# Optimization experiments

Measured on AMD Instinct MI355X. Metric: run time of the kernel, lower is better.

The kernel has to match this reference:

```python
import jax, jax.numpy as jnp
import numpy as np

B, C, D, H, W = 2, 256, 16, 64, 64


def _conv1x1(x, w, b):
    # 1x1x1 Conv3d == pointwise channel matmul. x: [B,C,D,H,W], w: [Cout,Cin], b: [Cout]
    return jnp.einsum('bcdhw,oc->bodhw', x, w) + b[None, :, None, None, None]


def setup_inputs() -> dict:
    key = jax.random.key(0)
    ks = jax.random.split(key, 12)
    wscale = 1.0 / np.sqrt(C)  # keep pre-softmax logits in a sane range
    inp = {
        'eeg_input': jax.random.normal(ks[0], (B, C, D, H, W), jnp.float32),
        'image_input': jax.random.normal(ks[1], (B, C, D, H, W), jnp.float32),
        'q_w': jax.random.normal(ks[2], (C, C), jnp.float32) * wscale,
        'q_b': jnp.zeros((C,), jnp.float32),
        'k_w': jax.random.normal(ks[3], (C, C), jnp.float32) * wscale,
        'k_b': jnp.zeros((C,), jnp.float32),
        'v_w': jax.random.normal(ks[4], (C, C), jnp.float32) * wscale,
        'v_b': jnp.zeros((C,), jnp.float32),
        'attn_w': jax.random.normal(ks[5], (C, C), jnp.float32) * wscale,
        'attn_b': jnp.zeros((C,), jnp.float32),
        'out_w': jax.random.normal(ks[6], (C, C), jnp.float32) * wscale,
        'out_b': jnp.zeros((C,), jnp.float32),
    }
    return inp


def reference(eeg_input, image_input, q_w, q_b, k_w, k_b, v_w, v_b,
              attn_w, attn_b, out_w, out_b):
    q = _conv1x1(eeg_input, q_w, q_b)      # [B,C,D,H,W]
    k = _conv1x1(image_input, k_w, k_b)    # [B,C,D,H,W]
    v = _conv1x1(image_input, v_w, v_b)    # [B,C,D,H,W]
    # torch.matmul(q, k.transpose(-2,-1)): contract over W -> scores [B,C,D,H,H]
    scores = jax.nn.softmax(jnp.einsum('bcdhw,bcdxw->bcdhx', q, k), axis=-1)
    wv = jnp.einsum('bcdhx,bcdxw->bcdhw', scores, v)  # [B,C,D,H,W]
    a = jax.nn.relu(_conv1x1(wv, attn_w, attn_b))
    return jax.nn.relu(_conv1x1(a, out_w, out_b))
```

## Files before the change

### kernel.cpp

```cpp
#include <hip/hip_runtime.h>

#define CC   256
#define DHWC 65536
#define NBC  2

typedef __attribute__((ext_vector_type(8))) short bf16x8;
typedef __attribute__((ext_vector_type(4))) short bf16x4;
typedef __attribute__((ext_vector_type(4))) float f32x4;

__device__ __forceinline__ short f2bf(float x) {
    unsigned u = __builtin_bit_cast(unsigned, x);
    unsigned r = (u + 0x7fffu + ((u >> 16) & 1u)) >> 16;
    return (short)r;
}
__device__ __forceinline__ float bf2f(short h) {
    unsigned u = ((unsigned)(unsigned short)h) << 16;
    return __builtin_bit_cast(float, u);
}

__device__ __forceinline__ int swz(int r, int c) {
    return (r * 128 + c * 2) ^ ((r & 7) << 4);
}
__device__ __forceinline__ int swz512(int s, int k) {
    return (s * 512 + k * 2) ^ ((s & 7) << 4);
}

__global__ void prep_w_kernel(const float* __restrict__ q_w, const float* __restrict__ k_w,
                              const float* __restrict__ v_w, const float* __restrict__ attn_w,
                              const float* __restrict__ out_w, short* __restrict__ wsp)
{
    const int l  = threadIdx.x;
    const int fo = blockIdx.x;
    const int t  = blockIdx.y;
    const int m  = blockIdx.z;
    const float* w = (m == 0) ? q_w : (m == 1) ? k_w : (m == 2) ? v_w
                   : (m == 3) ? attn_w : out_w;
    short* whi = wsp + (size_t)m * 2 * 65536;
    short* wlo = whi + 65536;

    const int o = fo * 16 + (l & 15);
    const int k = t * 32 + (l >> 4) * 8;

    bf16x8 hv, lv;
    #pragma unroll
    for (int r = 0; r < 8; ++r) {
        const float x = w[o * 256 + k + r];
        const short h = f2bf(x);
        hv[r] = h;
        lv[r] = f2bf(x - bf2f(h));
    }
    const int idx = (fo * 8 + t) * 64 + l;
    *(bf16x8*)(whi + idx * 8) = hv;
    *(bf16x8*)(wlo + idx * 8) = lv;
}

__global__ __launch_bounds__(512, 4) void conv_mfma_kernel(
    const float* __restrict__ x, const short* __restrict__ whi,
    const short* __restrict__ wlo, const float* __restrict__ bias,
    float* __restrict__ out, const int do_relu)
{
    __shared__ bf16x8 xhi[2][512];
    __shared__ bf16x8 xlo[2][512];

    const int tid  = threadIdx.x;
    const int lane = tid & 63;
    const int wave = tid >> 6;
    const size_t boff = (size_t)blockIdx.y * ((size_t)CC * DHWC);
    const int sT = blockIdx.x * 64;
    const float* xb = x + boff + sT;
    const bf16x8* whf = (const bf16x8*)whi;
    const bf16x8* wlf = (const bf16x8*)wlo;

    f32x4 acc[2][4];
    #pragma unroll
    for (int f = 0; f < 2; ++f)
        #pragma unroll
        for (int j = 0; j < 4; ++j)
            acc[f][j] = (f32x4){0.f, 0.f, 0.f, 0.f};

    const int s_l = tid & 63;
    const int k8  = tid >> 6;

    float xr[8];
    #pragma unroll
    for (int r = 0; r < 8; ++r)
        xr[r] = xb[(size_t)(k8 * 8 + r) * DHWC + s_l];
    {
        bf16x8 hv, lv;
        #pragma unroll
        for (int r = 0; r < 8; ++r) {
            const short h = f2bf(xr[r]);
            hv[r] = h;
            lv[r] = f2bf(xr[r] - bf2f(h));
        }
        *(bf16x8*)((char*)xhi[0] + swz(s_l, k8 * 8)) = hv;
        *(bf16x8*)((char*)xlo[0] + swz(s_l, k8 * 8)) = lv;
    }

    #pragma unroll
    for (int t = 0; t < 4; ++t) {
        if (t < 3) {
            #pragma unroll
            for (int r = 0; r < 8; ++r)
                xr[r] = xb[(size_t)((t + 1) * 64 + k8 * 8 + r) * DHWC + s_l];
        }
        __syncthreads();

        const char* bhib = (const char*)xhi[t & 1];
        const char* blob = (const char*)xlo[t & 1];
        #pragma unroll
        for (int kk = 0; kk < 2; ++kk) {
            bf16x8 a1h[2], a1l[2];
            #pragma unroll
            for (int f = 0; f < 2; ++f) {
                const int idx = ((wave * 2 + f) * 8 + 2 * t + kk) * 64 + lane;
                a1h[f] = whf[idx];
                a1l[f] = wlf[idx];
            }
            bf16x8 bh[4], bl[4];
            #pragma unroll
            for (int j = 0; j < 4; ++j) {
                const int s = j * 16 + (lane & 15);
                const int k = kk * 32 + (lane >> 4) * 8;
                bh[j] = *(const bf16x8*)(bhib + swz(s, k));
                bl[j] = *(const bf16x8*)(blob + swz(s, k));
            }
            #pragma unroll
            for (int f = 0; f < 2; ++f)
                #pragma unroll
                for (int j = 0; j < 4; ++j) {
                    f32x4 c = acc[f][j];
                    c = __builtin_amdgcn_mfma_f32_16x16x32_bf16(a1h[f], bh[j], c, 0, 0, 0);
                    c = __builtin_amdgcn_mfma_f32_16x16x32_bf16(a1h[f], bl[j], c, 0, 0, 0);
                    c = __builtin_amdgcn_mfma_f32_16x16x32_bf16(a1l[f], bh[j], c, 0, 0, 0);
                    acc[f][j] = c;
                }
        }

        if (t < 3) {
            bf16x8 hv, lv;
            #pragma unroll
            for (int r = 0; r < 8; ++r) {
                const short h = f2bf(xr[r]);
                hv[r] = h;
                lv[r] = f2bf(xr[r] - bf2f(h));
            }
            *(bf16x8*)((char*)xhi[(t + 1) & 1] + swz(s_l, k8 * 8)) = hv;
            *(bf16x8*)((char*)xlo[(t + 1) & 1] + swz(s_l, k8 * 8)) = lv;
        }
    }

    float* ob = out + boff + sT;
    const int n_l = lane & 15;
    const int m4  = (lane >> 4) * 4;
    #pragma unroll
    for (int f = 0; f < 2; ++f) {
        #pragma unroll
        for (int r = 0; r < 4; ++r) {
            const int o = wave * 32 + f * 16 + m4 + r;
            const float bv = bias[o];
            #pragma unroll
            for (int j = 0; j < 4; ++j) {
                float val = acc[f][j][r] + bv;
                if (do_relu) val = fmaxf(val, 0.f);
                ob[(size_t)o * DHWC + j * 16 + n_l] = val;
            }
        }
    }
}

__global__ __launch_bounds__(256, 4) void attn_mfma_kernel(
    const float* __restrict__ q, const float* __restrict__ kg,
    const float* __restrict__ v, float* __restrict__ wv)
{
    __shared__ char lds[40960];
    const int QHI = 0, QLO = 8192, KHI = 16384, KLO = 24576, VTHI = 32768;

    const int tid  = threadIdx.x;
    const int lane = tid & 63;
    const int wsx  = tid >> 6;
    const size_t base = (size_t)blockIdx.x * 4096;

    {
        const int r  = tid >> 2;
        const int cb = (tid & 3) * 16;
        #pragma unroll
        for (int half = 0; half < 2; ++half) {
            const int c = cb + half * 8;
            const float4 qa = *(const float4*)(q  + base + r * 64 + c);
            const float4 qb = *(const float4*)(q  + base + r * 64 + c + 4);
            const float4 ka = *(const float4*)(kg + base + r * 64 + c);
            const float4 kb = *(const float4*)(kg + base + r * 64 + c + 4);
            bf16x8 qh, ql, kh, kl;
            #pragma unroll
            for (int e = 0; e < 4; ++e) {
                float xq = ((const float*)&qa)[e];
                short h = f2bf(xq); qh[e] = h; ql[e] = f2bf(xq - bf2f(h));
                xq = ((const float*)&qb)[e];
                h = f2bf(xq); qh[e + 4] = h; ql[e + 4] = f2bf(xq - bf2f(h));
                float xk = ((const float*)&ka)[e];
                h = f2bf(xk); kh[e] = h; kl[e] = f2bf(xk - bf2f(h));
                xk = ((const float*)&kb)[e];
                h = f2bf(xk); kh[e + 4] = h; kl[e + 4] = f2bf(xk - bf2f(h));
            }
            const int off = swz(r, c);
            *(bf16x8*)(lds + QHI + off) = qh;
            *(bf16x8*)(lds + QLO + off) = ql;
            *(bf16x8*)(lds + KHI + off) = kh;
            *(bf16x8*)(lds + KLO + off) = kl;
        }
        const int x0 = (tid >> 4) * 4;
        const int w0 = (tid & 15) * 4;
        float4 vr[4];
        #pragma unroll
        for (int i = 0; i < 4; ++i)
            vr[i] = *(const float4*)(v + base + (size_t)(x0 + i) * 64 + w0);
        #pragma unroll
        for (int j = 0; j < 4; ++j) {
            bf16x4 h4;
            #pragma unroll
            for (int i = 0; i < 4; ++i)
                h4[i] = f2bf(((const float*)&vr[i])[j]);
            *(bf16x4*)(lds + VTHI + swz(w0 + j, x0)) = h4;
        }
    }
    __syncthreads();

    f32x4 acc[4];
    #pragma unroll
    for (int j = 0; j < 4; ++j) acc[j] = (f32x4){0.f, 0.f, 0.f, 0.f};

    const int arow = wsx * 16 + (lane & 15);
    #pragma unroll
    for (int kk = 0; kk < 2; ++kk) {
        const int kcol = kk * 32 + (lane >> 4) * 8;
        const bf16x8 aqh = *(const bf16x8*)(lds + QHI + swz(arow, kcol));
        const bf16x8 aql = *(const bf16x8*)(lds + QLO + swz(arow, kcol));
        #pragma unroll
        for (int j = 0; j < 4; ++j) {
            const int brow = j * 16 + (lane & 15);
            const bf16x8 bkh = *(const bf16x8*)(lds + KHI + swz(brow, kcol));
            const bf16x8 bkl = *(const bf16x8*)(lds + KLO + swz(brow, kcol));
            f32x4 c = acc[j];
            c = __builtin_amdgcn_mfma_f32_16x16x32_bf16(aqh, bkh, c, 0, 0, 0);
            c = __builtin_amdgcn_mfma_f32_16x16x32_bf16(aqh, bkl, c, 0, 0, 0);
            c = __builtin_amdgcn_mfma_f32_16x16x32_bf16(aql, bkh, c, 0, 0, 0);
            acc[j] = c;
        }
    }

    float p[4][4], invs[4];
    #pragma unroll
    for (int r = 0; r < 4; ++r) {
        float m = fmaxf(fmaxf(acc[0][r], acc[1][r]), fmaxf(acc[2][r], acc[3][r]));
        m = fmaxf(m, __shfl_xor(m, 1));
        m = fmaxf(m, __shfl_xor(m, 2));
        m = fmaxf(m, __shfl_xor(m, 4));
        m = fmaxf(m, __shfl_xor(m, 8));
        float s = 0.f;
        #pragma unroll
        for (int j = 0; j < 4; ++j) { p[j][r] = __expf(acc[j][r] - m); s += p[j][r]; }
        s += __shfl_xor(s, 1);
        s += __shfl_xor(s, 2);
        s += __shfl_xor(s, 4);
        s += __shfl_xor(s, 8);
        invs[r] = 1.f / s;
    }

    __syncthreads();

    #pragma unroll
    for (int r = 0; r < 4; ++r) {
        const int row = wsx * 16 + (lane >> 4) * 4 + r;
        #pragma unroll
        for (int j = 0; j < 4; ++j) {
            const int col = j * 16 + (lane & 15);
            *(short*)(lds + QHI + swz(row, col)) = f2bf(p[j][r]);
        }
    }
    __syncthreads();

    f32x4 o_[4];
    #pragma unroll
    for (int j = 0; j < 4; ++j) o_[j] = (f32x4){0.f, 0.f, 0.f, 0.f};

    #pragma unroll
    for (int kk = 0; kk < 2; ++kk) {
        const int kcol = kk * 32 + (lane >> 4) * 8;
        const bf16x8 aph = *(const bf16x8*)(lds + QHI + swz(arow, kcol));
        #pragma unroll
        for (int j = 0; j < 4; ++j) {
            const int brow = j * 16 + (lane & 15);
            const bf16x8 bvh = *(const bf16x8*)(lds + VTHI + swz(brow, kcol));
            o_[j] = __builtin_amdgcn_mfma_f32_16x16x32_bf16(aph, bvh, o_[j], 0, 0, 0);
        }
    }

    #pragma unroll
    for (int r = 0; r < 4; ++r) {
        const int h = wsx * 16 + (lane >> 4) * 4 + r;
        #pragma unroll
        for (int j = 0; j < 4; ++j)
            wv[base + (size_t)h * 64 + j * 16 + (lane & 15)] = o_[j][r] * invs[r];
    }
}

__global__ __launch_bounds__(512, 4) void tail_fused_kernel(
    const float* __restrict__ x,
    const short* __restrict__ w1hi, const short* __restrict__ w1lo,
    const float* __restrict__ b1,
    const short* __restrict__ w2hi, const short* __restrict__ w2lo,
    const float* __restrict__ b2,
    float* __restrict__ out)
{
    __shared__ char lds[65536];
    const int tid  = threadIdx.x;
    const int lane = tid & 63;
    const int wave = tid >> 6;
    const size_t boff = (size_t)blockIdx.y * ((size_t)CC * DHWC);
    const int sT = blockIdx.x * 64;
    const float* xb = x + boff + sT;
    const bf16x8* w1hf = (const bf16x8*)w1hi;
    const bf16x8* w1lf = (const bf16x8*)w1lo;

    f32x4 acc[2][4];
    #pragma unroll
    for (int f = 0; f < 2; ++f)
        #pragma unroll
        for (int j = 0; j < 4; ++j)
            acc[f][j] = (f32x4){0.f, 0.f, 0.f, 0.f};

    const int s_l = tid & 63;
    const int k8  = tid >> 6;

    float xr[8];
    #pragma unroll
    for (int r = 0; r < 8; ++r)
        xr[r] = xb[(size_t)(k8 * 8 + r) * DHWC + s_l];
    {
        bf16x8 hv, lv;
        #pragma unroll
        for (int r = 0; r < 8; ++r) {
            const short h = f2bf(xr[r]);
            hv[r] = h;
            lv[r] = f2bf(xr[r] - bf2f(h));
        }
        *(bf16x8*)(lds + swz(s_l, k8 * 8)) = hv;
        *(bf16x8*)(lds + 8192 + swz(s_l, k8 * 8)) = lv;
    }

    #pragma unroll
    for (int t = 0; t < 4; ++t) {
        if (t < 3) {
            #pragma unroll
            for (int r = 0; r < 8; ++r)
                xr[r] = xb[(size_t)((t + 1) * 64 + k8 * 8 + r) * DHWC + s_l];
        }
        __syncthreads();

        const char* bhib = lds + (t & 1) * 16384;
        const char* blob = bhib + 8192;
        #pragma unroll
        for (int kk = 0; kk < 2; ++kk) {
            bf16x8 a1h[2], a1l[2];
            #pragma unroll
            for (int f = 0; f < 2; ++f) {
                const int idx = ((wave * 2 + f) * 8 + 2 * t + kk) * 64 + lane;
                a1h[f] = w1hf[idx];
                a1l[f] = w1lf[idx];
            }
            bf16x8 bh[4], bl[4];
            #pragma unroll
            for (int j = 0; j < 4; ++j) {
                const int s = j * 16 + (lane & 15);
                const int k = kk * 32 + (lane >> 4) * 8;
                bh[j] = *(const bf16x8*)(bhib + swz(s, k));
                bl[j] = *(const bf16x8*)(blob + swz(s, k));
            }
            #pragma unroll
            for (int f = 0; f < 2; ++f)
                #pragma unroll
                for (int j = 0; j < 4; ++j) {
                    f32x4 c = acc[f][j];
                    c = __builtin_amdgcn_mfma_f32_16x16x32_bf16(a1h[f], bh[j], c, 0, 0, 0);
                    c = __builtin_amdgcn_mfma_f32_16x16x32_bf16(a1h[f], bl[j], c, 0, 0, 0);
                    c = __builtin_amdgcn_mfma_f32_16x16x32_bf16(a1l[f], bh[j], c, 0, 0, 0);
                    acc[f][j] = c;
                }
        }

        if (t < 3) {
            bf16x8 hv, lv;
            #pragma unroll
            for (int r = 0; r < 8; ++r) {
                const short h = f2bf(xr[r]);
                hv[r] = h;
                lv[r] = f2bf(xr[r] - bf2f(h));
            }
            *(bf16x8*)(lds + ((t + 1) & 1) * 16384 + swz(s_l, k8 * 8)) = hv;
            *(bf16x8*)(lds + ((t + 1) & 1) * 16384 + 8192 + swz(s_l, k8 * 8)) = lv;
        }
    }

    __syncthreads();
    #pragma unroll
    for (int f = 0; f < 2; ++f) {
        #pragma unroll
        for (int r = 0; r < 4; ++r) {
            const int o = wave * 32 + f * 16 + (lane >> 4) * 4 + r;
            const float bv = b1[o];
            #pragma unroll
            for (int j = 0; j < 4; ++j) {
                const int s = j * 16 + (lane & 15);
                const float val = fmaxf(acc[f][j][r] + bv, 0.f);
                const short h = f2bf(val);
                const int off = swz512(s, o);
                *(short*)(lds + off) = h;
                *(short*)(lds + 32768 + off) = f2bf(val - bf2f(h));
            }
        }
    }
    __syncthreads();

    f32x4 acc2[2][4];
    #pragma unroll
    for (int f = 0; f < 2; ++f)
        #pragma unroll
        for (int j = 0; j < 4; ++j)
            acc2[f][j] = (f32x4){0.f, 0.f, 0.f, 0.f};

    const bf16x8* w2hf = (const bf16x8*)w2hi;
    const bf16x8* w2lf = (const bf16x8*)w2lo;
    #pragma unroll
    for (int t2 = 0; t2 < 8; ++t2) {
        bf16x8 a2h[2], a2l[2];
        #pragma unroll
        for (int f = 0; f < 2; ++f) {
            const int idx = ((wave * 2 + f) * 8 + t2) * 64 + lane;
            a2h[f] = w2hf[idx];
            a2l[f] = w2lf[idx];
        }
        bf16x8 bh[4], bl[4];
        #pragma unroll
        for (int j = 0; j < 4; ++j) {
            const int s = j * 16 + (lane & 15);
            const int k = t2 * 32 + (lane >> 4) * 8;
            const int off = swz512(s, k);
            bh[j] = *(const bf16x8*)(lds + off);
            bl[j] = *(const bf16x8*)(lds + 32768 + off);
        }
        #pragma unroll
        for (int f = 0; f < 2; ++f)
            #pragma unroll
            for (int j = 0; j < 4; ++j) {
                f32x4 c = acc2[f][j];
                c = __builtin_amdgcn_mfma_f32_16x16x32_bf16(a2h[f], bh[j], c, 0, 0, 0);
                c = __builtin_amdgcn_mfma_f32_16x16x32_bf16(a2h[f], bl[j], c, 0, 0, 0);
                c = __builtin_amdgcn_mfma_f32_16x16x32_bf16(a2l[f], bh[j], c, 0, 0, 0);
                acc2[f][j] = c;
            }
    }

    float* ob = out + boff + sT;
    const int n_l = lane & 15;
    const int m4  = (lane >> 4) * 4;
    #pragma unroll
    for (int f = 0; f < 2; ++f) {
        #pragma unroll
        for (int r = 0; r < 4; ++r) {
            const int o = wave * 32 + f * 16 + m4 + r;
            const float bv = b2[o];
            #pragma unroll
            for (int j = 0; j < 4; ++j) {
                const float val = fmaxf(acc2[f][j][r] + bv, 0.f);
                ob[(size_t)o * DHWC + j * 16 + n_l] = val;
            }
        }
    }
}

extern "C" void kernel_launch(void* const* d_in, const int* in_sizes, int n_in,
                              void* d_out, int out_size, void* d_ws, size_t ws_size,
                              hipStream_t stream)
{
    const float* eeg    = (const float*)d_in[0];
    const float* img    = (const float*)d_in[1];
    const float* q_w    = (const float*)d_in[2];
    const float* q_b    = (const float*)d_in[3];
    const float* k_w    = (const float*)d_in[4];
    const float* k_b    = (const float*)d_in[5];
    const float* v_w    = (const float*)d_in[6];
    const float* v_b    = (const float*)d_in[7];
    const float* attn_w = (const float*)d_in[8];
    const float* attn_b = (const float*)d_in[9];
    const float* out_w  = (const float*)d_in[10];
    const float* out_b  = (const float*)d_in[11];

    float* outp = (float*)d_out;
    const size_t N = (size_t)NBC * CC * DHWC;
    float* qbuf = (float*)d_ws;
    float* kbuf = qbuf + N;
    short* wsp  = (short*)(kbuf + N);

    hipLaunchKernelGGL(prep_w_kernel, dim3(16, 8, 5), dim3(64), 0, stream,
                       q_w, k_w, v_w, attn_w, out_w, wsp);

    const dim3 cgrid(DHWC / 64, NBC);
    const dim3 cblk(512);
    #define WMAT(m) (wsp + (size_t)(m) * 2 * 65536), (wsp + (size_t)(m) * 2 * 65536 + 65536)

    hipLaunchKernelGGL(conv_mfma_kernel, cgrid, cblk, 0, stream, eeg,  WMAT(0), q_b, qbuf, 0);
    hipLaunchKernelGGL(conv_mfma_kernel, cgrid, cblk, 0, stream, img,  WMAT(1), k_b, kbuf, 0);
    hipLaunchKernelGGL(conv_mfma_kernel, cgrid, cblk, 0, stream, img,  WMAT(2), v_b, outp, 0);
    hipLaunchKernelGGL(attn_mfma_kernel, dim3(NBC * CC * 16), dim3(256), 0, stream,
                       qbuf, kbuf, outp, qbuf);
    hipLaunchKernelGGL(tail_fused_kernel, cgrid, cblk, 0, stream,
                       qbuf, WMAT(3), attn_b, WMAT(4), out_b, outp);
    #undef WMAT
}
```

Measured before the change: 438.8 us.

## Fuse QKV projections into one kernel and pass pre-split bf16 intermediates

The three separate conv kernels are merged into one qkv_kernel that stages each input tile in LDS once, so the image tile is shared between the K and V projections. Q and K are written as packed hi/lo bf16 pairs and V as plain bf16, which removes the float-to-bf16 splitting in the attention kernel and halves V traffic. The attention output is also written packed, so the tail kernel only unpacks it. In exchange, the non-double-buffered 64KB LDS staging lowers occupancy and loses the load/compute overlap the old conv kernels had. V is now stored at bf16 precision before attention, and the V transpose uses a new swizzle.

```diff
diff --git a/kernel.cpp b/kernel.cpp
--- a/kernel.cpp
+++ b/kernel.cpp
@@ -20,6 +20,9 @@
 
 __device__ __forceinline__ int swz(int r, int c) {
     return (r * 128 + c * 2) ^ ((r & 7) << 4);
+}
+__device__ __forceinline__ int vswz(int r, int c) {
+    return (r * 128 + c * 2) ^ (((r ^ (r >> 3)) & 7) << 4);
 }
 __device__ __forceinline__ int swz512(int s, int k) {
     return (s * 512 + k * 2) ^ ((s & 7) << 4);
@@ -35,7 +38,7 @@
     const int m  = blockIdx.z;
     const float* w = (m == 0) ? q_w : (m == 1) ? k_w : (m == 2) ? v_w
                    : (m == 3) ? attn_w : out_w;
-    short* whi = wsp + (size_t)m * 2 * 65536;
+    short* whi = wsp + (size_t)m * 131072;
     short* wlo = whi + 65536;
 
     const int o = fo * 16 + (l & 15);
@@ -54,127 +57,185 @@
     *(bf16x8*)(wlo + idx * 8) = lv;
 }
 
-__global__ __launch_bounds__(512, 4) void conv_mfma_kernel(
-    const float* __restrict__ x, const short* __restrict__ whi,
-    const short* __restrict__ wlo, const float* __restrict__ bias,
-    float* __restrict__ out, const int do_relu)
-{
-    __shared__ bf16x8 xhi[2][512];
-    __shared__ bf16x8 xlo[2][512];
-
+__device__ __forceinline__ void gemm256(const char* lds, const short* whi,
+                                        const short* wlo, int wave, int lane,
+                                        f32x4 acc[2][4])
+{
+    const bf16x8* whf = (const bf16x8*)whi;
+    const bf16x8* wlf = (const bf16x8*)wlo;
+    #pragma unroll
+    for (int t2 = 0; t2 < 8; ++t2) {
+        bf16x8 a2h[2], a2l[2];
+        #pragma unroll
+        for (int f = 0; f < 2; ++f) {
+            const int idx = ((wave * 2 + f) * 8 + t2) * 64 + lane;
+            a2h[f] = whf[idx];
+            a2l[f] = wlf[idx];
+        }
+        bf16x8 bh[4], bl[4];
+        #pragma unroll
+        for (int j = 0; j < 4; ++j) {
+            const int s = j * 16 + (lane & 15);
+            const int k = t2 * 32 + (lane >> 4) * 8;
+            const int off = swz512(s, k);
+            bh[j] = *(const bf16x8*)(lds + off);
+            bl[j] = *(const bf16x8*)(lds + 32768 + off);
+        }
+        #pragma unroll
+        for (int f = 0; f < 2; ++f)
+            #pragma unroll
+            for (int j = 0; j < 4; ++j) {
+                f32x4 c = acc[f][j];
+                c = __builtin_amdgcn_mfma_f32_16x16x32_bf16(a2h[f], bh[j], c, 0, 0, 0);
+                c = __builtin_amdgcn_mfma_f32_16x16x32_bf16(a2h[f], bl[j], c, 0, 0, 0);
+                c = __builtin_amdgcn_mfma_f32_16x16x32_bf16(a2l[f], bh[j], c, 0, 0, 0);
+                acc[f][j] = c;
+            }
+    }
+}
+
+__device__ __forceinline__ void stage_f32(const float* xb, char* lds, int tid)
+{
+    const int s_l = tid & 63;
+    const int k8  = tid >> 6;
+    #pragma unroll
+    for (int t = 0; t < 4; ++t) {
+        float xr[8];
+        #pragma unroll
+        for (int r = 0; r < 8; ++r)
+            xr[r] = xb[(size_t)(t * 64 + k8 * 8 + r) * DHWC + s_l];
+        bf16x8 hv, lv;
+        #pragma unroll
+        for (int r = 0; r < 8; ++r) {
+            const short h = f2bf(xr[r]);
+            hv[r] = h;
+            lv[r] = f2bf(xr[r] - bf2f(h));
+        }
+        const int off = swz512(s_l, t * 64 + k8 * 8);
+        *(bf16x8*)(lds + off) = hv;
+        *(bf16x8*)(lds + 32768 + off) = lv;
+    }
+}
+
+__device__ __forceinline__ void stage_u32(const unsigned* xb, char* lds, int tid)
+{
+    const int s_l = tid & 63;
+    const int k8  = tid >> 6;
+    #pragma unroll
+    for (int t = 0; t < 4; ++t) {
+        unsigned xu[8];
+        #pragma unroll
+        for (int r = 0; r < 8; ++r)
+            xu[r] = xb[(size_t)(t * 64 + k8 * 8 + r) * DHWC + s_l];
+        bf16x8 hv, lv;
+        #pragma unroll
+        for (int r = 0; r < 8; ++r) {
+            hv[r] = (short)(xu[r] & 0xffffu);
+            lv[r] = (short)(xu[r] >> 16);
+        }
+        const int off = swz512(s_l, t * 64 + k8 * 8);
+        *(bf16x8*)(lds + off) = hv;
+        *(bf16x8*)(lds + 32768 + off) = lv;
+    }
+}
+
+__global__ __launch_bounds__(512, 4) void qkv_kernel(
+    const float* __restrict__ eeg, const float* __restrict__ img,
+    const short* __restrict__ wsp,
+    const float* __restrict__ qb, const float* __restrict__ kb,
+    const float* __restrict__ vb,
+    unsigned* __restrict__ qout, unsigned* __restrict__ kout,
+    short* __restrict__ vout)
+{
+    __shared__ char lds[65536];
     const int tid  = threadIdx.x;
     const int lane = tid & 63;
     const int wave = tid >> 6;
     const size_t boff = (size_t)blockIdx.y * ((size_t)CC * DHWC);
     const int sT = blockIdx.x * 64;
-    const float* xb = x + boff + sT;
-    const bf16x8* whf = (const bf16x8*)whi;
-    const bf16x8* wlf = (const bf16x8*)wlo;
+    const int n_l = lane & 15;
+    const int m4  = (lane >> 4) * 4;
 
     f32x4 acc[2][4];
+
+    stage_f32(eeg + boff + sT, lds, tid);
+    __syncthreads();
     #pragma unroll
     for (int f = 0; f < 2; ++f)
         #pragma unroll
-        for (int j = 0; j < 4; ++j)
-            acc[f][j] = (f32x4){0.f, 0.f, 0.f, 0.f};
-
-    const int s_l = tid & 63;
-    const int k8  = tid >> 6;
-
-    float xr[8];
-    #pragma unroll
-    for (int r = 0; r < 8; ++r)
-        xr[r] = xb[(size_t)(k8 * 8 + r) * DHWC + s_l];
+        for (int j = 0; j < 4; ++j) acc[f][j] = (f32x4){0.f, 0.f, 0.f, 0.f};
+    gemm256(lds, wsp, wsp + 65536, wave, lane, acc);
     {
-        bf16x8 hv, lv;
-        #pragma unroll
-        for (int r = 0; r < 8; ++r) {
-            const short h = f2bf(xr[r]);
-            hv[r] = h;
-            lv[r] = f2bf(xr[r] - bf2f(h));
-        }
-        *(bf16x8*)((char*)xhi[0] + swz(s_l, k8 * 8)) = hv;
-        *(bf16x8*)((char*)xlo[0] + swz(s_l, k8 * 8)) = lv;
-    }
-
-    #pragma unroll
-    for (int t = 0; t < 4; ++t) {
-        if (t < 3) {
-            #pragma unroll
-            for (int r = 0; r < 8; ++r)
-                xr[r] = xb[(size_t)((t + 1) * 64 + k8 * 8 + r) * DHWC + s_l];
-        }
-        __syncthreads();
-
-        const char* bhib = (const char*)xhi[t & 1];
-        const char* blob = (const char*)xlo[t & 1];
-        #pragma unroll
-        for (int kk = 0; kk < 2; ++kk) {
-            bf16x8 a1h[2], a1l[2];
-            #pragma unroll
-            for (int f = 0; f < 2; ++f) {
-                const int idx = ((wave * 2 + f) * 8 + 2 * t + kk) * 64 + lane;
-                a1h[f] = whf[idx];
-                a1l[f] = wlf[idx];
-            }
-            bf16x8 bh[4], bl[4];
-            #pragma unroll
-            for (int j = 0; j < 4; ++j) {
-                const int s = j * 16 + (lane & 15);
-                const int k = kk * 32 + (lane >> 4) * 8;
-                bh[j] = *(const bf16x8*)(bhib + swz(s, k));
-                bl[j] = *(const bf16x8*)(blob + swz(s, k));
-            }
-            #pragma unroll
-            for (int f = 0; f < 2; ++f)
+        unsigned* qo = qout + boff + sT;
+        #pragma unroll
+        for (int f = 0; f < 2; ++f)
+            #pragma unroll
+            for (int r = 0; r < 4; ++r) {
+                const int o = wave * 32 + f * 16 + m4 + r;
+                const float bv = qb[o];
                 #pragma unroll
                 for (int j = 0; j < 4; ++j) {
-                    f32x4 c = acc[f][j];
-                    c = __builtin_amdgcn_mfma_f32_16x16x32_bf16(a1h[f], bh[j], c, 0, 0, 0);
-                    c = __builtin_amdgcn_mfma_f32_16x16x32_bf16(a1h[f], bl[j], c, 0, 0, 0);
-                    c = __builtin_amdgcn_mfma_f32_16x16x32_bf16(a1l[f], bh[j], c, 0, 0, 0);
-                    acc[f][j] = c;
+                    const float val = acc[f][j][r] + bv;
+                    const short h = f2bf(val);
+                    const short l = f2bf(val - bf2f(h));
+                    qo[(size_t)o * DHWC + j * 16 + n_l] =
+                        (unsigned)(unsigned short)h | ((unsigned)(unsigned short)l << 16);
                 }
-        }
-
-        if (t < 3) {
-            bf16x8 hv, lv;
-            #pragma unroll
-            for (int r = 0; r < 8; ++r) {
-                const short h = f2bf(xr[r]);
-                hv[r] = h;
-                lv[r] = f2bf(xr[r] - bf2f(h));
             }
-            *(bf16x8*)((char*)xhi[(t + 1) & 1] + swz(s_l, k8 * 8)) = hv;
-            *(bf16x8*)((char*)xlo[(t + 1) & 1] + swz(s_l, k8 * 8)) = lv;
-        }
-    }
-
-    float* ob = out + boff + sT;
-    const int n_l = lane & 15;
-    const int m4  = (lane >> 4) * 4;
-    #pragma unroll
-    for (int f = 0; f < 2; ++f) {
-        #pragma unroll
-        for (int r = 0; r < 4; ++r) {
-            const int o = wave * 32 + f * 16 + m4 + r;
-            const float bv = bias[o];
-            #pragma unroll
-            for (int j = 0; j < 4; ++j) {
-                float val = acc[f][j][r] + bv;
-                if (do_relu) val = fmaxf(val, 0.f);
-                ob[(size_t)o * DHWC + j * 16 + n_l] = val;
+    }
+    __syncthreads();
+
+    stage_f32(img + boff + sT, lds, tid);
+    __syncthreads();
+    #pragma unroll
+    for (int f = 0; f < 2; ++f)
+        #pragma unroll
+        for (int j = 0; j < 4; ++j) acc[f][j] = (f32x4){0.f, 0.f, 0.f, 0.f};
+    gemm256(lds, wsp + 131072, wsp + 131072 + 65536, wave, lane, acc);
+    {
+        unsigned* ko = kout + boff + sT;
+        #pragma unroll
+        for (int f = 0; f < 2; ++f)
+            #pragma unroll
+            for (int r = 0; r < 4; ++r) {
+                const int o = wave * 32 + f * 16 + m4 + r;
+                const float bv = kb[o];
+                #pragma unroll
+                for (int j = 0; j < 4; ++j) {
+                    const float val = acc[f][j][r] + bv;
+                    const short h = f2bf(val);
+                    const short l = f2bf(val - bf2f(h));
+                    ko[(size_t)o * DHWC + j * 16 + n_l] =
+                        (unsigned)(unsigned short)h | ((unsigned)(unsigned short)l << 16);
+                }
             }
-        }
+    }
+    #pragma unroll
+    for (int f = 0; f < 2; ++f)
+        #pragma unroll
+        for (int j = 0; j < 4; ++j) acc[f][j] = (f32x4){0.f, 0.f, 0.f, 0.f};
+    gemm256(lds, wsp + 2 * 131072, wsp + 2 * 131072 + 65536, wave, lane, acc);
+    {
+        short* vo = vout + boff + sT;
+        #pragma unroll
+        for (int f = 0; f < 2; ++f)
+            #pragma unroll
+            for (int r = 0; r < 4; ++r) {
+                const int o = wave * 32 + f * 16 + m4 + r;
+                const float bv = vb[o];
+                #pragma unroll
+                for (int j = 0; j < 4; ++j)
+                    vo[(size_t)o * DHWC + j * 16 + n_l] = f2bf(acc[f][j][r] + bv);
+            }
     }
 }
 
 __global__ __launch_bounds__(256, 4) void attn_mfma_kernel(
-    const float* __restrict__ q, const float* __restrict__ kg,
-    const float* __restrict__ v, float* __restrict__ wv)
+    const unsigned* __restrict__ qpk, unsigned* kpk,
+    const short* __restrict__ vsh)
 {
     __shared__ char lds[40960];
-    const int QHI = 0, QLO = 8192, KHI = 16384, KLO = 24576, VTHI = 32768;
+    const int QHI = 0, QLO = 8192, KHI = 16384, KLO = 24576, VT = 32768;
 
     const int tid  = threadIdx.x;
     const int lane = tid & 63;
@@ -182,46 +243,42 @@
     const size_t base = (size_t)blockIdx.x * 4096;
 
     {
-        const int r  = tid >> 2;
-        const int cb = (tid & 3) * 16;
-        #pragma unroll
-        for (int half = 0; half < 2; ++half) {
-            const int c = cb + half * 8;
-            const float4 qa = *(const float4*)(q  + base + r * 64 + c);
-            const float4 qb = *(const float4*)(q  + base + r * 64 + c + 4);
-            const float4 ka = *(const float4*)(kg + base + r * 64 + c);
-            const float4 kb = *(const float4*)(kg + base + r * 64 + c + 4);
-            bf16x8 qh, ql, kh, kl;
-            #pragma unroll
-            for (int e = 0; e < 4; ++e) {
-                float xq = ((const float*)&qa)[e];
-                short h = f2bf(xq); qh[e] = h; ql[e] = f2bf(xq - bf2f(h));
-                xq = ((const float*)&qb)[e];
-                h = f2bf(xq); qh[e + 4] = h; ql[e + 4] = f2bf(xq - bf2f(h));
-                float xk = ((const float*)&ka)[e];
-                h = f2bf(xk); kh[e] = h; kl[e] = f2bf(xk - bf2f(h));
-                xk = ((const float*)&kb)[e];
-                h = f2bf(xk); kh[e + 4] = h; kl[e + 4] = f2bf(xk - bf2f(h));
-            }
-            const int off = swz(r, c);
-            *(bf16x8*)(lds + QHI + off) = qh;
-            *(bf16x8*)(lds + QLO + off) = ql;
-            *(bf16x8*)(lds + KHI + off) = kh;
-            *(bf16x8*)(lds + KLO + off) = kl;
-        }
+        const unsigned* qpl = qpk + base;
+        const unsigned* kpl = kpk + base;
+        #pragma unroll
+        for (int it = 0; it < 4; ++it) {
+            const int e = it * 1024 + tid * 4;
+            const int h = e >> 6, w = e & 63;
+            const uint4 qu = *(const uint4*)(qpl + e);
+            const uint4 ku = *(const uint4*)(kpl + e);
+            bf16x4 qh4, ql4, kh4, kl4;
+            qh4[0] = (short)qu.x; ql4[0] = (short)(qu.x >> 16);
+            qh4[1] = (short)qu.y; ql4[1] = (short)(qu.y >> 16);
+            qh4[2] = (short)qu.z; ql4[2] = (short)(qu.z >> 16);
+            qh4[3] = (short)qu.w; ql4[3] = (short)(qu.w >> 16);
+            kh4[0] = (short)ku.x; kl4[0] = (short)(ku.x >> 16);
+            kh4[1] = (short)ku.y; kl4[1] = (short)(ku.y >> 16);
+            kh4[2] = (short)ku.z; kl4[2] = (short)(ku.z >> 16);
+            kh4[3] = (short)ku.w; kl4[3] = (short)(ku.w >> 16);
+            const int off = swz(h, w);
+            *(bf16x4*)(lds + QHI + off) = qh4;
+            *(bf16x4*)(lds + QLO + off) = ql4;
+            *(bf16x4*)(lds + KHI + off) = kh4;
+            *(bf16x4*)(lds + KLO + off) = kl4;
+        }
+        const short* vpl = vsh + base;
         const int x0 = (tid >> 4) * 4;
         const int w0 = (tid & 15) * 4;
-        float4 vr[4];
+        bf16x4 vr[4];
         #pragma unroll
         for (int i = 0; i < 4; ++i)
-            vr[i] = *(const float4*)(v + base + (size_t)(x0 + i) * 64 + w0);
-        #pragma unroll
-        for (int j = 0; j < 4; ++j) {
-            bf16x4 h4;
-            #pragma unroll
-            for (int i = 0; i < 4; ++i)
-                h4[i] = f2bf(((const float*)&vr[i])[j]);
-            *(bf16x4*)(lds + VTHI + swz(w0 + j, x0)) = h4;
+            vr[i] = *(const bf16x4*)(vpl + (x0 + i) * 64 + w0);
+        #pragma unroll
+        for (int j = 0; j < 4; ++j) {
+            bf16x4 tv;
+            #pragma unroll
+            for (int i = 0; i < 4; ++i) tv[i] = vr[i][j];
+            *(bf16x4*)(lds + VT + vswz(w0 + j, x0)) = tv;
         }
     }
     __syncthreads();
@@ -291,7 +348,7 @@
         #pragma unroll
         for (int j = 0; j < 4; ++j) {
             const int brow = j * 16 + (lane & 15);
-            const bf16x8 bvh = *(const bf16x8*)(lds + VTHI + swz(brow, kcol));
+            const bf16x8 bvh = *(const bf16x8*)(lds + VT + vswz(brow, kcol));
             o_[j] = __builtin_amdgcn_mfma_f32_16x16x32_bf16(aph, bvh, o_[j], 0, 0, 0);
         }
     }
@@ -300,17 +357,20 @@
     for (int r = 0; r < 4; ++r) {
         const int h = wsx * 16 + (lane >> 4) * 4 + r;
         #pragma unroll
-        for (int j = 0; j < 4; ++j)
-            wv[base + (size_t)h * 64 + j * 16 + (lane & 15)] = o_[j][r] * invs[r];
+        for (int j = 0; j < 4; ++j) {
+            const float val = o_[j][r] * invs[r];
+            const short hh = f2bf(val);
+            const short ll = f2bf(val - bf2f(hh));
+            kpk[base + (size_t)h * 64 + j * 16 + (lane & 15)] =
+                (unsigned)(unsigned short)hh | ((unsigned)(unsigned short)ll << 16);
+        }
     }
 }
 
 __global__ __launch_bounds__(512, 4) void tail_fused_kernel(
-    const float* __restrict__ x,
-    const short* __restrict__ w1hi, const short* __restrict__ w1lo,
-    const float* __restrict__ b1,
-    const short* __restrict__ w2hi, const short* __restrict__ w2lo,
-    const float* __restrict__ b2,
+    const unsigned* __restrict__ xpk,
+    const short* __restrict__ wsp,
+    const float* __restrict__ b1, const float* __restrict__ b2,
     float* __restrict__ out)
 {
     __shared__ char lds[65536];
@@ -319,90 +379,20 @@
     const int wave = tid >> 6;
     const size_t boff = (size_t)blockIdx.y * ((size_t)CC * DHWC);
     const int sT = blockIdx.x * 64;
-    const float* xb = x + boff + sT;
-    const bf16x8* w1hf = (const bf16x8*)w1hi;
-    const bf16x8* w1lf = (const bf16x8*)w1lo;
+    const int n_l = lane & 15;
+    const int m4  = (lane >> 4) * 4;
 
     f32x4 acc[2][4];
+
+    stage_u32(xpk + boff + sT, lds, tid);
+    __syncthreads();
     #pragma unroll
     for (int f = 0; f < 2; ++f)
         #pragma unroll
-        for (int j = 0; j < 4; ++j)
-            acc[f][j] = (f32x4){0.f, 0.f, 0.f, 0.f};
-
-    const int s_l = tid & 63;
-    const int k8  = tid >> 6;
-
-    float xr[8];
-    #pragma unroll
-    for (int r = 0; r < 8; ++r)
-        xr[r] = xb[(size_t)(k8 * 8 + r) * DHWC + s_l];
-    {
-        bf16x8 hv, lv;
-        #pragma unroll
-        for (int r = 0; r < 8; ++r) {
-            const short h = f2bf(xr[r]);
-            hv[r] = h;
-            lv[r] = f2bf(xr[r] - bf2f(h));
-        }
-        *(bf16x8*)(lds + swz(s_l, k8 * 8)) = hv;
-        *(bf16x8*)(lds + 8192 + swz(s_l, k8 * 8)) = lv;
-    }
-
-    #pragma unroll
-    for (int t = 0; t < 4; ++t) {
-        if (t < 3) {
-            #pragma unroll
-            for (int r = 0; r < 8; ++r)
-                xr[r] = xb[(size_t)((t + 1) * 64 + k8 * 8 + r) * DHWC + s_l];
-        }
-        __syncthreads();
-
-        const char* bhib = lds + (t & 1) * 16384;
-        const char* blob = bhib + 8192;
-        #pragma unroll
-        for (int kk = 0; kk < 2; ++kk) {
-            bf16x8 a1h[2], a1l[2];
-            #pragma unroll
-            for (int f = 0; f < 2; ++f) {
-                const int idx = ((wave * 2 + f) * 8 + 2 * t + kk) * 64 + lane;
-                a1h[f] = w1hf[idx];
-                a1l[f] = w1lf[idx];
-            }
-            bf16x8 bh[4], bl[4];
-            #pragma unroll
-            for (int j = 0; j < 4; ++j) {
-                const int s = j * 16 + (lane & 15);
-                const int k = kk * 32 + (lane >> 4) * 8;
-                bh[j] = *(const bf16x8*)(bhib + swz(s, k));
-                bl[j] = *(const bf16x8*)(blob + swz(s, k));
-            }
-            #pragma unroll
-            for (int f = 0; f < 2; ++f)
-                #pragma unroll
-                for (int j = 0; j < 4; ++j) {
-                    f32x4 c = acc[f][j];
-                    c = __builtin_amdgcn_mfma_f32_16x16x32_bf16(a1h[f], bh[j], c, 0, 0, 0);
-                    c = __builtin_amdgcn_mfma_f32_16x16x32_bf16(a1h[f], bl[j], c, 0, 0, 0);
-                    c = __builtin_amdgcn_mfma_f32_16x16x32_bf16(a1l[f], bh[j], c, 0, 0, 0);
-                    acc[f][j] = c;
-                }
-        }
-
-        if (t < 3) {
-            bf16x8 hv, lv;
-            #pragma unroll
-            for (int r = 0; r < 8; ++r) {
-                const short h = f2bf(xr[r]);
-                hv[r] = h;
-                lv[r] = f2bf(xr[r] - bf2f(h));
-            }
-            *(bf16x8*)(lds + ((t + 1) & 1) * 16384 + swz(s_l, k8 * 8)) = hv;
-            *(bf16x8*)(lds + ((t + 1) & 1) * 16384 + 8192 + swz(s_l, k8 * 8)) = lv;
-        }
-    }
-
-    __syncthreads();
+        for (int j = 0; j < 4; ++j) acc[f][j] = (f32x4){0.f, 0.f, 0.f, 0.f};
+    gemm256(lds, wsp + 3 * 131072, wsp + 3 * 131072 + 65536, wave, lane, acc);
+    __syncthreads();
+
     #pragma unroll
     for (int f = 0; f < 2; ++f) {
         #pragma unroll
@@ -422,48 +412,13 @@
     }
     __syncthreads();
 
-    f32x4 acc2[2][4];
     #pragma unroll
     for (int f = 0; f < 2; ++f)
         #pragma unroll
-        for (int j = 0; j < 4; ++j)
-            acc2[f][j] = (f32x4){0.f, 0.f, 0.f, 0.f};
-
-    const bf16x8* w2hf = (const bf16x8*)w2hi;
-    const bf16x8* w2lf = (const bf16x8*)w2lo;
-    #pragma unroll
-    for (int t2 = 0; t2 < 8; ++t2) {
-        bf16x8 a2h[2], a2l[2];
-        #pragma unroll
-        for (int f = 0; f < 2; ++f) {
-            const int idx = ((wave * 2 + f) * 8 + t2) * 64 + lane;
-            a2h[f] = w2hf[idx];
-            a2l[f] = w2lf[idx];
-        }
-        bf16x8 bh[4], bl[4];
-        #pragma unroll
-        for (int j = 0; j < 4; ++j) {
-            const int s = j * 16 + (lane & 15);
-            const int k = t2 * 32 + (lane >> 4) * 8;
-            const int off = swz512(s, k);
-            bh[j] = *(const bf16x8*)(lds + off);
-            bl[j] = *(const bf16x8*)(lds + 32768 + off);
-        }
-        #pragma unroll
-        for (int f = 0; f < 2; ++f)
-            #pragma unroll
-            for (int j = 0; j < 4; ++j) {
-                f32x4 c = acc2[f][j];
-                c = __builtin_amdgcn_mfma_f32_16x16x32_bf16(a2h[f], bh[j], c, 0, 0, 0);
-                c = __builtin_amdgcn_mfma_f32_16x16x32_bf16(a2h[f], bl[j], c, 0, 0, 0);
-                c = __builtin_amdgcn_mfma_f32_16x16x32_bf16(a2l[f], bh[j], c, 0, 0, 0);
-                acc2[f][j] = c;
-            }
-    }
+        for (int j = 0; j < 4; ++j) acc[f][j] = (f32x4){0.f, 0.f, 0.f, 0.f};
+    gemm256(lds, wsp + 4 * 131072, wsp + 4 * 131072 + 65536, wave, lane, acc);
 
     float* ob = out + boff + sT;
-    const int n_l = lane & 15;
-    const int m4  = (lane >> 4) * 4;
     #pragma unroll
     for (int f = 0; f < 2; ++f) {
         #pragma unroll
@@ -471,10 +426,8 @@
             const int o = wave * 32 + f * 16 + m4 + r;
             const float bv = b2[o];
             #pragma unroll
-            for (int j = 0; j < 4; ++j) {
-                const float val = fmaxf(acc2[f][j][r] + bv, 0.f);
-                ob[(size_t)o * DHWC + j * 16 + n_l] = val;
-            }
+            for (int j = 0; j < 4; ++j)
+                ob[(size_t)o * DHWC + j * 16 + n_l] = fmaxf(acc[f][j][r] + bv, 0.f);
         }
     }
 }
@@ -496,25 +449,22 @@
     const float* out_w  = (const float*)d_in[10];
     const float* out_b  = (const float*)d_in[11];
 
-    float* outp = (float*)d_out;
     const size_t N = (size_t)NBC * CC * DHWC;
-    float* qbuf = (float*)d_ws;
-    float* kbuf = qbuf + N;
-    short* wsp  = (short*)(kbuf + N);
+    unsigned* qpk = (unsigned*)d_ws;
+    unsigned* kpk = qpk + N;
+    short*    wsp = (short*)(kpk + N);
+    short*    vsh = (short*)d_out;
+    float*    outp = (float*)d_out;
 
     hipLaunchKernelGGL(prep_w_kernel, dim3(16, 8, 5), dim3(64), 0, stream,
                        q_w, k_w, v_w, attn_w, out_w, wsp);
 
-    const dim3 cgrid(DHWC / 64, NBC);
-    const dim3 cblk(512);
-    #define WMAT(m) (wsp + (size_t)(m) * 2 * 65536), (wsp + (size_t)(m) * 2 * 65536 + 65536)
-
-    hipLaunchKernelGGL(conv_mfma_kernel, cgrid, cblk, 0, stream, eeg,  WMAT(0), q_b, qbuf, 0);
-    hipLaunchKernelGGL(conv_mfma_kernel, cgrid, cblk, 0, stream, img,  WMAT(1), k_b, kbuf, 0);
-    hipLaunchKernelGGL(conv_mfma_kernel, cgrid, cblk, 0, stream, img,  WMAT(2), v_b, outp, 0);
+    hipLaunchKernelGGL(qkv_kernel, dim3(DHWC / 64, NBC), dim3(512), 0, stream,
+                       eeg, img, wsp, q_b, k_b, v_b, qpk, kpk, vsh);
+
     hipLaunchKernelGGL(attn_mfma_kernel, dim3(NBC * CC * 16), dim3(256), 0, stream,
-                       qbuf, kbuf, outp, qbuf);
-    hipLaunchKernelGGL(tail_fused_kernel, cgrid, cblk, 0, stream,
-                       qbuf, WMAT(3), attn_b, WMAT(4), out_b, outp);
-    #undef WMAT
-}
+                       qpk, kpk, vsh);
+
+    hipLaunchKernelGGL(tail_fused_kernel, dim3(DHWC / 64, NBC), dim3(512), 0, stream,
+                       kpk, wsp, attn_b, out_b, outp);
+}
```

Result: slower. 534.8 us (+21.9%).

## Fuse K and V projections into one kernel and store V as bf16

Applied to the files above, without the earlier changes.

The separate K and V 1x1 convolutions are merged into one kernel that reads the image input once and computes both projections with shared B-operand tiles. V is written directly as bf16 into the output buffer, so the attention kernel reads half the bytes and skips its own conversion. A new LDS swizzle is used for the transposed V tile. The cost is higher register pressure from doubled accumulators in the fused kernel.

```diff
diff --git a/kernel.cpp b/kernel.cpp
--- a/kernel.cpp
+++ b/kernel.cpp
@@ -20,6 +20,9 @@
 
 __device__ __forceinline__ int swz(int r, int c) {
     return (r * 128 + c * 2) ^ ((r & 7) << 4);
+}
+__device__ __forceinline__ int vswz(int r, int c) {
+    return (r * 128 + c * 2) ^ (((r ^ (r >> 3)) & 7) << 4);
 }
 __device__ __forceinline__ int swz512(int s, int k) {
     return (s * 512 + k * 2) ^ ((s & 7) << 4);
@@ -35,7 +38,7 @@
     const int m  = blockIdx.z;
     const float* w = (m == 0) ? q_w : (m == 1) ? k_w : (m == 2) ? v_w
                    : (m == 3) ? attn_w : out_w;
-    short* whi = wsp + (size_t)m * 2 * 65536;
+    short* whi = wsp + (size_t)m * 131072;
     short* wlo = whi + 65536;
 
     const int o = fo * 16 + (l & 15);
@@ -169,12 +172,138 @@
     }
 }
 
+__global__ __launch_bounds__(512, 4) void kv_conv_kernel(
+    const float* __restrict__ img,
+    const short* __restrict__ wkhi, const short* __restrict__ wklo,
+    const short* __restrict__ wvhi, const short* __restrict__ wvlo,
+    const float* __restrict__ kb, const float* __restrict__ vb,
+    float* __restrict__ kout, short* __restrict__ vout)
+{
+    __shared__ bf16x8 xhi[2][512];
+    __shared__ bf16x8 xlo[2][512];
+
+    const int tid  = threadIdx.x;
+    const int lane = tid & 63;
+    const int wave = tid >> 6;
+    const size_t boff = (size_t)blockIdx.y * ((size_t)CC * DHWC);
+    const int sT = blockIdx.x * 64;
+    const float* xb = img + boff + sT;
+    const bf16x8* wkhf = (const bf16x8*)wkhi;
+    const bf16x8* wklf = (const bf16x8*)wklo;
+    const bf16x8* wvhf = (const bf16x8*)wvhi;
+    const bf16x8* wvlf = (const bf16x8*)wvlo;
+
+    f32x4 acck[2][4], accv[2][4];
+    #pragma unroll
+    for (int f = 0; f < 2; ++f)
+        #pragma unroll
+        for (int j = 0; j < 4; ++j) {
+            acck[f][j] = (f32x4){0.f, 0.f, 0.f, 0.f};
+            accv[f][j] = (f32x4){0.f, 0.f, 0.f, 0.f};
+        }
+
+    const int s_l = tid & 63;
+    const int k8  = tid >> 6;
+
+    float xr[8];
+    #pragma unroll
+    for (int r = 0; r < 8; ++r)
+        xr[r] = xb[(size_t)(k8 * 8 + r) * DHWC + s_l];
+    {
+        bf16x8 hv, lv;
+        #pragma unroll
+        for (int r = 0; r < 8; ++r) {
+            const short h = f2bf(xr[r]);
+            hv[r] = h;
+            lv[r] = f2bf(xr[r] - bf2f(h));
+        }
+        *(bf16x8*)((char*)xhi[0] + swz(s_l, k8 * 8)) = hv;
+        *(bf16x8*)((char*)xlo[0] + swz(s_l, k8 * 8)) = lv;
+    }
+
+    #pragma unroll
+    for (int t = 0; t < 4; ++t) {
+        if (t < 3) {
+            #pragma unroll
+            for (int r = 0; r < 8; ++r)
+                xr[r] = xb[(size_t)((t + 1) * 64 + k8 * 8 + r) * DHWC + s_l];
+        }
+        __syncthreads();
+
+        const char* bhib = (const char*)xhi[t & 1];
+        const char* blob = (const char*)xlo[t & 1];
+        #pragma unroll
+        for (int kk = 0; kk < 2; ++kk) {
+            bf16x8 akh[2], akl[2], avh[2], avl[2];
+            #pragma unroll
+            for (int f = 0; f < 2; ++f) {
+                const int idx = ((wave * 2 + f) * 8 + 2 * t + kk) * 64 + lane;
+                akh[f] = wkhf[idx];
+                akl[f] = wklf[idx];
+                avh[f] = wvhf[idx];
+                avl[f] = wvlf[idx];
+            }
+            #pragma unroll
+            for (int j = 0; j < 4; ++j) {
+                const int s = j * 16 + (lane & 15);
+                const int k = kk * 32 + (lane >> 4) * 8;
+                const bf16x8 bh = *(const bf16x8*)(bhib + swz(s, k));
+                const bf16x8 bl = *(const bf16x8*)(blob + swz(s, k));
+                #pragma unroll
+                for (int f = 0; f < 2; ++f) {
+                    f32x4 c = acck[f][j];
+                    c = __builtin_amdgcn_mfma_f32_16x16x32_bf16(akh[f], bh, c, 0, 0, 0);
+                    c = __builtin_amdgcn_mfma_f32_16x16x32_bf16(akh[f], bl, c, 0, 0, 0);
+                    c = __builtin_amdgcn_mfma_f32_16x16x32_bf16(akl[f], bh, c, 0, 0, 0);
+                    acck[f][j] = c;
+                    f32x4 d = accv[f][j];
+                    d = __builtin_amdgcn_mfma_f32_16x16x32_bf16(avh[f], bh, d, 0, 0, 0);
+                    d = __builtin_amdgcn_mfma_f32_16x16x32_bf16(avh[f], bl, d, 0, 0, 0);
+                    d = __builtin_amdgcn_mfma_f32_16x16x32_bf16(avl[f], bh, d, 0, 0, 0);
+                    accv[f][j] = d;
+                }
+            }
+        }
+
+        if (t < 3) {
+            bf16x8 hv, lv;
+            #pragma unroll
+            for (int r = 0; r < 8; ++r) {
+                const short h = f2bf(xr[r]);
+                hv[r] = h;
+                lv[r] = f2bf(xr[r] - bf2f(h));
+            }
+            *(bf16x8*)((char*)xhi[(t + 1) & 1] + swz(s_l, k8 * 8)) = hv;
+            *(bf16x8*)((char*)xlo[(t + 1) & 1] + swz(s_l, k8 * 8)) = lv;
+        }
+    }
+
+    float* ko = kout + boff + sT;
+    short* vo = vout + boff + sT;
+    const int n_l = lane & 15;
+    const int m4  = (lane >> 4) * 4;
+    #pragma unroll
+    for (int f = 0; f < 2; ++f) {
+        #pragma unroll
+        for (int r = 0; r < 4; ++r) {
+            const int o = wave * 32 + f * 16 + m4 + r;
+            const float kbv = kb[o];
+            const float vbv = vb[o];
+            #pragma unroll
+            for (int j = 0; j < 4; ++j) {
+                ko[(size_t)o * DHWC + j * 16 + n_l] = acck[f][j][r] + kbv;
+                vo[(size_t)o * DHWC + j * 16 + n_l] = f2bf(accv[f][j][r] + vbv);
+            }
+        }
+    }
+}
+
 __global__ __launch_bounds__(256, 4) void attn_mfma_kernel(
-    const float* __restrict__ q, const float* __restrict__ kg,
-    const float* __restrict__ v, float* __restrict__ wv)
+    const float* q, const float* __restrict__ kg,
+    const short* __restrict__ vsh, float* wv)
 {
     __shared__ char lds[40960];
-    const int QHI = 0, QLO = 8192, KHI = 16384, KLO = 24576, VTHI = 32768;
+    const int QHI = 0, QLO = 8192, KHI = 16384, KLO = 24576, VT = 32768;
 
     const int tid  = threadIdx.x;
     const int lane = tid & 63;
@@ -209,19 +338,19 @@
             *(bf16x8*)(lds + KHI + off) = kh;
             *(bf16x8*)(lds + KLO + off) = kl;
         }
+        const short* vpl = vsh + base;
         const int x0 = (tid >> 4) * 4;
         const int w0 = (tid & 15) * 4;
-        float4 vr[4];
+        bf16x4 vr[4];
         #pragma unroll
         for (int i = 0; i < 4; ++i)
-            vr[i] = *(const float4*)(v + base + (size_t)(x0 + i) * 64 + w0);
+            vr[i] = *(const bf16x4*)(vpl + (x0 + i) * 64 + w0);
         #pragma unroll
         for (int j = 0; j < 4; ++j) {
-            bf16x4 h4;
-            #pragma unroll
-            for (int i = 0; i < 4; ++i)
-                h4[i] = f2bf(((const float*)&vr[i])[j]);
-            *(bf16x4*)(lds + VTHI + swz(w0 + j, x0)) = h4;
+            bf16x4 tv;
+            #pragma unroll
+            for (int i = 0; i < 4; ++i) tv[i] = vr[i][j];
+            *(bf16x4*)(lds + VT + vswz(w0 + j, x0)) = tv;
         }
     }
     __syncthreads();
@@ -291,7 +420,7 @@
         #pragma unroll
         for (int j = 0; j < 4; ++j) {
             const int brow = j * 16 + (lane & 15);
-            const bf16x8 bvh = *(const bf16x8*)(lds + VTHI + swz(brow, kcol));
+            const bf16x8 bvh = *(const bf16x8*)(lds + VT + vswz(brow, kcol));
             o_[j] = __builtin_amdgcn_mfma_f32_16x16x32_bf16(aph, bvh, o_[j], 0, 0, 0);
         }
     }
@@ -496,25 +625,30 @@
     const float* out_w  = (const float*)d_in[10];
     const float* out_b  = (const float*)d_in[11];
 
-    float* outp = (float*)d_out;
     const size_t N = (size_t)NBC * CC * DHWC;
     float* qbuf = (float*)d_ws;
     float* kbuf = qbuf + N;
     short* wsp  = (short*)(kbuf + N);
+    short* vsh  = (short*)d_out;
+    float* outp = (float*)d_out;
 
     hipLaunchKernelGGL(prep_w_kernel, dim3(16, 8, 5), dim3(64), 0, stream,
                        q_w, k_w, v_w, attn_w, out_w, wsp);
 
     const dim3 cgrid(DHWC / 64, NBC);
-    const dim3 cblk(512);
-    #define WMAT(m) (wsp + (size_t)(m) * 2 * 65536), (wsp + (size_t)(m) * 2 * 65536 + 65536)
-
-    hipLaunchKernelGGL(conv_mfma_kernel, cgrid, cblk, 0, stream, eeg,  WMAT(0), q_b, qbuf, 0);
-    hipLaunchKernelGGL(conv_mfma_kernel, cgrid, cblk, 0, stream, img,  WMAT(1), k_b, kbuf, 0);
-    hipLaunchKernelGGL(conv_mfma_kernel, cgrid, cblk, 0, stream, img,  WMAT(2), v_b, outp, 0);
+
+    hipLaunchKernelGGL(conv_mfma_kernel, cgrid, dim3(512), 0, stream,
+                       eeg, wsp, wsp + 65536, q_b, qbuf, 0);
+
+    hipLaunchKernelGGL(kv_conv_kernel, cgrid, dim3(512), 0, stream,
+                       img, wsp + 131072, wsp + 131072 + 65536,
+                       wsp + 2 * 131072, wsp + 2 * 131072 + 65536,
+                       k_b, v_b, kbuf, vsh);
+
     hipLaunchKernelGGL(attn_mfma_kernel, dim3(NBC * CC * 16), dim3(256), 0, stream,
-                       qbuf, kbuf, outp, qbuf);
-    hipLaunchKernelGGL(tail_fused_kernel, cgrid, cblk, 0, stream,
-                       qbuf, WMAT(3), attn_b, WMAT(4), out_b, outp);
-    #undef WMAT
-}
+                       qbuf, kbuf, vsh, qbuf);
+
+    hipLaunchKernelGGL(tail_fused_kernel, cgrid, dim3(512), 0, stream,
+                       qbuf, wsp + 3 * 131072, wsp + 3 * 131072 + 65536, attn_b,
+                       wsp + 4 * 131072, wsp + 4 * 131072 + 65536, out_b, outp);
+}
```

Result: faster. 417.4 us (-4.9%).
